# Kernel tuning notes

Measured on AMD Instinct MI355X. Metric: run time of the kernel, lower is better.

Reference implementation:

```python
import jax, jax.numpy as jnp
import numpy as np

QMAX = 127.0  # symmetric int8 fake quantization

def fake_quant(t):
    # per-tensor symmetric int8 fake quant: scale = max|t|/127
    scale = jnp.max(jnp.abs(t)) / QMAX
    scale = jnp.maximum(scale, 1e-8)
    q = jnp.clip(jnp.round(t / scale), -QMAX, QMAX)
    return q * scale

def setup_inputs() -> dict:
    key = jax.random.key(0)
    k1, k2, k3 = jax.random.split(key, 3)
    B, S, D_IN, D_OUT = 8, 2048, 4096, 4096
    x = jax.random.normal(k1, (B, S, D_IN), dtype=jnp.float32)
    # kaiming_uniform-like init scale
    bound = np.sqrt(6.0 / D_IN)
    weights = jax.random.uniform(k2, (D_OUT, D_IN), dtype=jnp.float32, minval=-bound, maxval=bound)
    stdv = 1.0 / np.sqrt(D_IN)
    bias = jax.random.uniform(k3, (D_OUT,), dtype=jnp.float32, minval=-stdv, maxval=stdv)
    return {"x": x, "weights": weights, "bias": bias}

def reference(x, weights, bias):
    x_q = fake_quant(x)          # quantize activations
    w_q = fake_quant(weights)    # quantize weights
    # F.linear: x @ W^T + b
    return jnp.einsum('bsi,oi->bso', x_q, w_q) + bias
```

## Files before the change

kernel.cpp:

```cpp
#include <hip/hip_runtime.h>
#include <hip/hip_bf16.h>
#include <cstddef>
#include <cstdint>


typedef int i32x4 __attribute__((ext_vector_type(4)));

__device__ __forceinline__ void async16(const void* g, void* l) {
    __builtin_amdgcn_global_load_lds(
        (const __attribute__((address_space(1))) void*)g,
        (__attribute__((address_space(3))) void*)l,
        16, 0, 0);
}

__global__ void absmax_kernel(const float* __restrict__ in, unsigned int n4,
                              unsigned int* __restrict__ out_bits) {
    const float4* in4 = (const float4*)in;
    float m = 0.0f;
    for (unsigned int i = blockIdx.x * blockDim.x + threadIdx.x; i < n4;
         i += gridDim.x * blockDim.x) {
        float4 v = in4[i];
        m = fmaxf(m, fmaxf(fmaxf(fabsf(v.x), fabsf(v.y)),
                           fmaxf(fabsf(v.z), fabsf(v.w))));
    }
    #pragma unroll
    for (int o = 32; o > 0; o >>= 1)
        m = fmaxf(m, __shfl_xor(m, o));
    __shared__ float wmax[8];
    int lane = threadIdx.x & 63;
    int wv = threadIdx.x >> 6;
    if (lane == 0) wmax[wv] = m;
    __syncthreads();
    if (threadIdx.x == 0) {
        int nw = blockDim.x >> 6;
        float b = wmax[0];
        for (int i = 1; i < nw; ++i) b = fmaxf(b, wmax[i]);
        atomicMax(out_bits, __float_as_uint(b));
    }
}

__global__ void quant_kernel(const float* __restrict__ in, char* __restrict__ out,
                             unsigned int n4,
                             const unsigned int* __restrict__ absmax_bits) {
    float s = fmaxf(__uint_as_float(*absmax_bits) / 127.0f, 1e-8f);
    const float4* in4 = (const float4*)in;
    char4* out4 = (char4*)out;
    for (unsigned int i = blockIdx.x * blockDim.x + threadIdx.x; i < n4;
         i += gridDim.x * blockDim.x) {
        float4 v = in4[i];
        char4 q;
        q.x = (char)(int)fminf(fmaxf(rintf(v.x / s), -127.0f), 127.0f);
        q.y = (char)(int)fminf(fmaxf(rintf(v.y / s), -127.0f), 127.0f);
        q.z = (char)(int)fminf(fmaxf(rintf(v.z / s), -127.0f), 127.0f);
        q.w = (char)(int)fminf(fmaxf(rintf(v.w / s), -127.0f), 127.0f);
        out4[i] = q;
    }
}

#define BM 128
#define BN 128
#define BK 64

__global__ __launch_bounds__(256) void gemm_i8_kernel(
    const char* __restrict__ Aq, const char* __restrict__ Bq,
    const float* __restrict__ bias, float* __restrict__ C,
    const unsigned int* __restrict__ scale_bits, int M, int N, int K) {
    __shared__ char sA[BM * BK];
    __shared__ char sB[BN * BK];

    const int t = threadIdx.x;
    const int lane = t & 63;
    const int wave = t >> 6;
    const int wm = wave >> 1;
    const int wn = wave & 1;

    const int m0 = blockIdx.y * BM;
    const int n0 = blockIdx.x * BN;

    const int ar = t >> 2;
    const int ac = (t & 3) * 16;

    const char* gA0 = Aq + (size_t)(m0 + ar) * K + ac;
    const char* gA1 = Aq + (size_t)(m0 + ar + 64) * K + ac;
    const char* gB0 = Bq + (size_t)(n0 + ar) * K + ac;
    const char* gB1 = Bq + (size_t)(n0 + ar + 64) * K + ac;

    i32x4 acc[4][4] = {};

    const int lr = lane & 15;
    const int kg = lane >> 4;

    for (int k0 = 0; k0 < K; k0 += BK) {
        async16(gA0 + k0, sA + t * 16);
        async16(gA1 + k0, sA + (t + 256) * 16);
        async16(gB0 + k0, sB + t * 16);
        async16(gB1 + k0, sB + (t + 256) * 16);
        __syncthreads();

        i32x4 af[4], bf[4];
        #pragma unroll
        for (int i = 0; i < 4; ++i) {
            af[i] = *(const i32x4*)(sA + (wm * 64 + i * 16 + lr) * BK + kg * 16);
            bf[i] = *(const i32x4*)(sB + (wn * 64 + i * 16 + lr) * BK + kg * 16);
        }
        #pragma unroll
        for (int i = 0; i < 4; ++i)
            #pragma unroll
            for (int j = 0; j < 4; ++j)
                acc[i][j] = __builtin_amdgcn_mfma_i32_16x16x64_i8(
                    af[i], bf[j], acc[i][j], 0, 0, 0);
        __syncthreads();
    }

    float sx = fmaxf(__uint_as_float(scale_bits[0]) / 127.0f, 1e-8f);
    float sw = fmaxf(__uint_as_float(scale_bits[1]) / 127.0f, 1e-8f);
    float s = sx * sw;

    #pragma unroll
    for (int i = 0; i < 4; ++i) {
        int row = m0 + wm * 64 + i * 16 + kg * 4;
        #pragma unroll
        for (int j = 0; j < 4; ++j) {
            int col = n0 + wn * 64 + j * 16 + lr;
            float bv = bias[col];
            float* Cp = C + (size_t)row * N + col;
            #pragma unroll
            for (int r = 0; r < 4; ++r)
                Cp[(size_t)r * N] = (float)acc[i][j][r] * s + bv;
        }
    }
}

extern "C" void kernel_launch(void* const* d_in, const int* in_sizes, int n_in,
                              void* d_out, int out_size, void* d_ws, size_t ws_size,
                              hipStream_t stream) {
    const float* x = (const float*)d_in[0];
    const float* w = (const float*)d_in[1];
    const float* bias = (const float*)d_in[2];
    float* out = (float*)d_out;

    const int N = in_sizes[2];
    const int K = in_sizes[1] / N;
    const int M = in_sizes[0] / K;

    unsigned int* scale_bits = (unsigned int*)d_ws;
    char* xq = (char*)d_ws + 256;
    char* wq = xq + (size_t)M * K;

    const unsigned int nx4 = (unsigned int)((size_t)M * K / 4);
    const unsigned int nw4 = (unsigned int)((size_t)N * K / 4);

    hipMemsetAsync(d_ws, 0, 16, stream);

    absmax_kernel<<<2048, 256, 0, stream>>>(x, nx4, scale_bits + 0);
    absmax_kernel<<<1024, 256, 0, stream>>>(w, nw4, scale_bits + 1);

    quant_kernel<<<2048, 256, 0, stream>>>(x, xq, nx4, scale_bits + 0);
    quant_kernel<<<1024, 256, 0, stream>>>(w, wq, nw4, scale_bits + 1);

    dim3 grid(N / BN, M / BM);
    gemm_i8_kernel<<<grid, 256, 0, stream>>>(xq, wq, bias, out, scale_bits, M, N, K);
}
```

Baseline: 933.4 us.

## Pipeline int8 GEMM with 4-stage LDS ring, 256x256 tiles and swizzle

The int8 GEMM is rebuilt around 256x256 tiles and 8 waves, each computing a 128x64 sub-tile. Global-to-LDS async loads now run through a 4-deep ring buffer, with explicit vmcnt waits, split A/B prefetch and setprio around the MFMA bursts. An XOR swizzle on LDS columns is added to avoid bank conflicts. The quant kernel is also widened to write 16 bytes per thread. The aim is to hide load latency and raise MFMA utilisation, at the cost of 128KB of LDS, higher register pressure and fragile hand-written waitcnt logic.

After: 828.7 us. 11.2% less time.

```diff
diff --git a/kernel.cpp b/kernel.cpp
--- a/kernel.cpp
+++ b/kernel.cpp
@@ -1,5 +1,4 @@
 #include <hip/hip_runtime.h>
-#include <hip/hip_bf16.h>
 #include <cstddef>
 #include <cstdint>
 
@@ -39,94 +38,155 @@
     }
 }
 
+__device__ __forceinline__ int quant4(float4 v, float s) {
+    int a = (int)fminf(fmaxf(rintf(v.x / s), -127.0f), 127.0f);
+    int b = (int)fminf(fmaxf(rintf(v.y / s), -127.0f), 127.0f);
+    int c = (int)fminf(fmaxf(rintf(v.z / s), -127.0f), 127.0f);
+    int d = (int)fminf(fmaxf(rintf(v.w / s), -127.0f), 127.0f);
+    return (a & 255) | ((b & 255) << 8) | ((c & 255) << 16) | (d << 24);
+}
+
 __global__ void quant_kernel(const float* __restrict__ in, char* __restrict__ out,
-                             unsigned int n4,
+                             unsigned int n16,
                              const unsigned int* __restrict__ absmax_bits) {
     float s = fmaxf(__uint_as_float(*absmax_bits) / 127.0f, 1e-8f);
     const float4* in4 = (const float4*)in;
-    char4* out4 = (char4*)out;
-    for (unsigned int i = blockIdx.x * blockDim.x + threadIdx.x; i < n4;
+    i32x4* out16 = (i32x4*)out;
+    for (unsigned int i = blockIdx.x * blockDim.x + threadIdx.x; i < n16;
          i += gridDim.x * blockDim.x) {
-        float4 v = in4[i];
-        char4 q;
-        q.x = (char)(int)fminf(fmaxf(rintf(v.x / s), -127.0f), 127.0f);
-        q.y = (char)(int)fminf(fmaxf(rintf(v.y / s), -127.0f), 127.0f);
-        q.z = (char)(int)fminf(fmaxf(rintf(v.z / s), -127.0f), 127.0f);
-        q.w = (char)(int)fminf(fmaxf(rintf(v.w / s), -127.0f), 127.0f);
-        out4[i] = q;
-    }
-}
-
-#define BM 128
-#define BN 128
-#define BK 64
-
-__global__ __launch_bounds__(256) void gemm_i8_kernel(
+        float4 v0 = in4[i * 4 + 0];
+        float4 v1 = in4[i * 4 + 1];
+        float4 v2 = in4[i * 4 + 2];
+        float4 v3 = in4[i * 4 + 3];
+        i32x4 q;
+        q[0] = quant4(v0, s);
+        q[1] = quant4(v1, s);
+        q[2] = quant4(v2, s);
+        q[3] = quant4(v3, s);
+        out16[i] = q;
+    }
+}
+
+#define BM 256
+#define BN 256
+
+__global__ __launch_bounds__(512, 2) void gemm_i8_kernel(
     const char* __restrict__ Aq, const char* __restrict__ Bq,
     const float* __restrict__ bias, float* __restrict__ C,
     const unsigned int* __restrict__ scale_bits, int M, int N, int K) {
-    __shared__ char sA[BM * BK];
-    __shared__ char sB[BN * BK];
+    __shared__ char lds[4 * 16384 * 2];
+    char* const sA = lds;
+    char* const sB = lds + 4 * 16384;
 
     const int t = threadIdx.x;
     const int lane = t & 63;
-    const int wave = t >> 6;
-    const int wm = wave >> 1;
-    const int wn = wave & 1;
+    const int w = t >> 6;
+    const int wm = w >> 2;
+    const int wn = w & 3;
 
     const int m0 = blockIdx.y * BM;
     const int n0 = blockIdx.x * BN;
 
-    const int ar = t >> 2;
-    const int ac = (t & 3) * 16;
-
-    const char* gA0 = Aq + (size_t)(m0 + ar) * K + ac;
-    const char* gA1 = Aq + (size_t)(m0 + ar + 64) * K + ac;
-    const char* gB0 = Bq + (size_t)(n0 + ar) * K + ac;
-    const char* gB1 = Bq + (size_t)(n0 + ar + 64) * K + ac;
-
-    i32x4 acc[4][4] = {};
-
-    const int lr = lane & 15;
-    const int kg = lane >> 4;
-
-    for (int k0 = 0; k0 < K; k0 += BK) {
-        async16(gA0 + k0, sA + t * 16);
-        async16(gA1 + k0, sA + (t + 256) * 16);
-        async16(gB0 + k0, sB + t * 16);
-        async16(gB1 + k0, sB + (t + 256) * 16);
-        __syncthreads();
-
-        i32x4 af[4], bf[4];
-        #pragma unroll
-        for (int i = 0; i < 4; ++i) {
-            af[i] = *(const i32x4*)(sA + (wm * 64 + i * 16 + lr) * BK + kg * 16);
-            bf[i] = *(const i32x4*)(sB + (wn * 64 + i * 16 + lr) * BK + kg * 16);
+    const int sr = t >> 2;
+    const int scl = (t & 3) ^ ((t >> 3) & 3);
+    const char* gA0 = Aq + (size_t)(m0 + sr) * K + scl * 16;
+    const char* gA1 = Aq + (size_t)(m0 + sr + 128) * K + scl * 16;
+    const char* gB0 = Bq + (size_t)(n0 + sr) * K + scl * 16;
+    const char* gB1 = Bq + (size_t)(n0 + sr + 128) * K + scl * 16;
+
+#define STAGE_A(kt) do { char* d_ = sA + ((kt) & 3) * 16384 + t * 16;          \
+        size_t ko_ = (size_t)(kt) * 64;                                        \
+        async16(gA0 + ko_, d_); async16(gA1 + ko_, d_ + 8192); } while (0)
+#define STAGE_B(kt) do { char* d_ = sB + ((kt) & 3) * 16384 + t * 16;          \
+        size_t ko_ = (size_t)(kt) * 64;                                        \
+        async16(gB0 + ko_, d_); async16(gB1 + ko_, d_ + 8192); } while (0)
+
+    const int rl = lane & 15;
+    const int cg = lane >> 4;
+    const int csw = (cg ^ ((rl >> 1) & 3)) << 4;
+    const int aoff = wm * 8192 + rl * 64 + csw;
+    const int boff = wn * 4096 + rl * 64 + csw;
+
+    i32x4 acc[8][4] = {};
+
+    const int NT = K >> 6;
+
+    STAGE_A(0); STAGE_B(0);
+    STAGE_A(1); STAGE_B(1);
+    STAGE_A(2); STAGE_B(2);
+    asm volatile("s_waitcnt vmcnt(8)" ::: "memory");
+    __builtin_amdgcn_s_barrier();
+
+#define MFMA_ROW(ai, AF)                                                        \
+    acc[ai][0] = __builtin_amdgcn_mfma_i32_16x16x64_i8(AF, bf0, acc[ai][0], 0, 0, 0); \
+    acc[ai][1] = __builtin_amdgcn_mfma_i32_16x16x64_i8(AF, bf1, acc[ai][1], 0, 0, 0); \
+    acc[ai][2] = __builtin_amdgcn_mfma_i32_16x16x64_i8(AF, bf2, acc[ai][2], 0, 0, 0); \
+    acc[ai][3] = __builtin_amdgcn_mfma_i32_16x16x64_i8(AF, bf3, acc[ai][3], 0, 0, 0);
+
+    for (int kt = 0; kt < NT; ++kt) {
+        const char* cA = sA + (kt & 3) * 16384;
+        const char* cB = sB + (kt & 3) * 16384;
+
+        i32x4 af0 = *(const i32x4*)(cA + aoff);
+        i32x4 af1 = *(const i32x4*)(cA + aoff + 1024);
+        i32x4 af2 = *(const i32x4*)(cA + aoff + 2048);
+        i32x4 af3 = *(const i32x4*)(cA + aoff + 3072);
+        i32x4 bf0 = *(const i32x4*)(cB + boff);
+        i32x4 bf1 = *(const i32x4*)(cB + boff + 1024);
+        i32x4 bf2 = *(const i32x4*)(cB + boff + 2048);
+        i32x4 bf3 = *(const i32x4*)(cB + boff + 3072);
+        if (kt + 3 < NT) STAGE_A(kt + 3);
+        __builtin_amdgcn_s_barrier();
+        asm volatile("s_waitcnt lgkmcnt(0)" ::: "memory");
+        __builtin_amdgcn_sched_barrier(0);
+        __builtin_amdgcn_s_setprio(1);
+        MFMA_ROW(0, af0)
+        MFMA_ROW(1, af1)
+        MFMA_ROW(2, af2)
+        MFMA_ROW(3, af3)
+        __builtin_amdgcn_s_setprio(0);
+        __builtin_amdgcn_s_barrier();
+
+        af0 = *(const i32x4*)(cA + aoff + 4096);
+        af1 = *(const i32x4*)(cA + aoff + 5120);
+        af2 = *(const i32x4*)(cA + aoff + 6144);
+        af3 = *(const i32x4*)(cA + aoff + 7168);
+        if (kt + 3 < NT) STAGE_B(kt + 3);
+        __builtin_amdgcn_s_barrier();
+        asm volatile("s_waitcnt lgkmcnt(0)" ::: "memory");
+        __builtin_amdgcn_sched_barrier(0);
+        __builtin_amdgcn_s_setprio(1);
+        MFMA_ROW(4, af0)
+        MFMA_ROW(5, af1)
+        MFMA_ROW(6, af2)
+        MFMA_ROW(7, af3)
+        __builtin_amdgcn_s_setprio(0);
+        if (kt < NT - 3) {
+            asm volatile("s_waitcnt vmcnt(8)" ::: "memory");
+        } else if (kt == NT - 3) {
+            asm volatile("s_waitcnt vmcnt(4)" ::: "memory");
+        } else if (kt == NT - 2) {
+            asm volatile("s_waitcnt vmcnt(0)" ::: "memory");
         }
-        #pragma unroll
-        for (int i = 0; i < 4; ++i)
-            #pragma unroll
-            for (int j = 0; j < 4; ++j)
-                acc[i][j] = __builtin_amdgcn_mfma_i32_16x16x64_i8(
-                    af[i], bf[j], acc[i][j], 0, 0, 0);
-        __syncthreads();
+        __builtin_amdgcn_s_barrier();
     }
 
     float sx = fmaxf(__uint_as_float(scale_bits[0]) / 127.0f, 1e-8f);
     float sw = fmaxf(__uint_as_float(scale_bits[1]) / 127.0f, 1e-8f);
     float s = sx * sw;
 
+    const int crow = m0 + wm * 128 + cg * 4;
+    const int ccol = n0 + wn * 64 + rl;
     #pragma unroll
-    for (int i = 0; i < 4; ++i) {
-        int row = m0 + wm * 64 + i * 16 + kg * 4;
+    for (int nt = 0; nt < 4; ++nt) {
+        int col = ccol + nt * 16;
+        float bv = bias[col];
         #pragma unroll
-        for (int j = 0; j < 4; ++j) {
-            int col = n0 + wn * 64 + j * 16 + lr;
-            float bv = bias[col];
-            float* Cp = C + (size_t)row * N + col;
+        for (int mt = 0; mt < 8; ++mt) {
+            float* Cp = C + (size_t)(crow + mt * 16) * N + col;
             #pragma unroll
             for (int r = 0; r < 4; ++r)
-                Cp[(size_t)r * N] = (float)acc[i][j][r] * s + bv;
+                Cp[(size_t)r * N] = (float)acc[mt][nt][r] * s + bv;
         }
     }
 }
@@ -149,15 +209,17 @@
 
     const unsigned int nx4 = (unsigned int)((size_t)M * K / 4);
     const unsigned int nw4 = (unsigned int)((size_t)N * K / 4);
+    const unsigned int nx16 = nx4 / 4;
+    const unsigned int nw16 = nw4 / 4;
 
     hipMemsetAsync(d_ws, 0, 16, stream);
 
     absmax_kernel<<<2048, 256, 0, stream>>>(x, nx4, scale_bits + 0);
     absmax_kernel<<<1024, 256, 0, stream>>>(w, nw4, scale_bits + 1);
 
-    quant_kernel<<<2048, 256, 0, stream>>>(x, xq, nx4, scale_bits + 0);
-    quant_kernel<<<1024, 256, 0, stream>>>(w, wq, nw4, scale_bits + 1);
+    quant_kernel<<<2048, 256, 0, stream>>>(x, xq, nx16, scale_bits + 0);
+    quant_kernel<<<1024, 256, 0, stream>>>(w, wq, nw16, scale_bits + 1);
 
     dim3 grid(N / BN, M / BM);
-    gemm_i8_kernel<<<grid, 256, 0, stream>>>(xq, wq, bias, out, scale_bits, M, N, K);
-}
+    gemm_i8_kernel<<<grid, 512, 0, stream>>>(xq, wq, bias, out, scale_bits, M, N, K);
+}
```
